# Optimization experiments

Hardware: AMD Instinct MI355X
Metric: run time of the kernel (lower is better)

The kernel has to match this reference:

```python
import jax, jax.numpy as jnp
import numpy as np

NQ = 10
C64 = jnp.complex64

# ---- gate matrices (built from traced fp32 params) ----

def u3(t, p, d):
    c = jnp.cos(t * 0.5).astype(C64)
    s = jnp.sin(t * 0.5).astype(C64)
    ep = jnp.exp(1j * p.astype(C64))
    ed = jnp.exp(1j * d.astype(C64))
    return jnp.stack([jnp.stack([c, -ed * s]), jnp.stack([ep * s, ep * ed * c])])

def ry(t):
    c = jnp.cos(t * 0.5).astype(C64)
    s = jnp.sin(t * 0.5).astype(C64)
    return jnp.stack([jnp.stack([c, -s]), jnp.stack([s, c])])

def rz(t):
    e = jnp.exp(-0.5j * t.astype(C64))
    ep = jnp.exp(0.5j * t.astype(C64))
    return jnp.diag(jnp.stack([e, ep]))

def rx(t):
    c = jnp.cos(t * 0.5).astype(C64)
    s = jnp.sin(t * 0.5).astype(C64)
    return jnp.stack([jnp.stack([c, -1j * s]), jnp.stack([-1j * s, c])])

def crz(t):
    one = jnp.ones((), C64)
    return jnp.diag(jnp.stack([one, one, jnp.exp(-0.5j * t.astype(C64)), jnp.exp(0.5j * t.astype(C64))]))

def crx(t):
    return jnp.eye(4, dtype=C64).at[2:, 2:].set(rx(t))

X = jnp.array([[0, 1], [1, 0]], dtype=C64)
CNOT = jnp.array([[1, 0, 0, 0], [0, 1, 0, 0], [0, 0, 0, 1], [0, 0, 1, 0]], dtype=C64)

# ---- gate application on state of shape (B, 2,...,2) ----

def ap1(st, U, w):
    ax = 1 + w
    s = jnp.moveaxis(st, ax, -1)
    s = s @ U.T
    return jnp.moveaxis(s, -1, ax)

def ap2(st, U, a, b):
    s = jnp.moveaxis(st, (1 + a, 1 + b), (-2, -1))
    sh = s.shape
    s = s.reshape(sh[:-2] + (4,)) @ U.T
    return jnp.moveaxis(s.reshape(sh), (-2, -1), (1 + a, 1 + b))

def conv_block(st, w, a, b):
    st = ap1(st, u3(w[0], w[1], w[2]), a)
    st = ap1(st, u3(w[3], w[4], w[5]), b)
    st = ap2(st, CNOT, a, b)
    st = ap1(st, ry(w[6]), a)
    st = ap1(st, rz(w[7]), b)
    st = ap2(st, CNOT, b, a)
    st = ap1(st, ry(w[8]), a)
    st = ap2(st, CNOT, a, b)
    st = ap1(st, u3(w[9], w[10], w[11]), a)
    st = ap1(st, u3(w[12], w[13], w[14]), b)
    return st

def pool_block(st, p, c, t):
    st = ap2(st, crz(p[0]), c, t)
    st = ap1(st, X, c)
    st = ap2(st, crx(p[1]), c, t)
    return st

def zexp(st, w):
    p = jnp.abs(st) ** 2  # fp32
    axes = tuple(ax for ax in range(1, NQ + 1) if ax != 1 + w)
    pz = p.sum(axis=axes)  # (B, 2)
    return pz[:, 0] - pz[:, 1]


def setup_inputs() -> dict:
    key = jax.random.key(0)
    ks = jax.random.split(key, 6)
    two_pi = 2.0 * np.pi
    return {
        "x": jax.random.normal(ks[0], (16384, 1024), dtype=jnp.float32),
        "weights_conv1": jax.random.uniform(ks[1], (10, 15), jnp.float32) * two_pi,
        "weights_conv2": jax.random.uniform(ks[2], (4, 15), jnp.float32) * two_pi,
        "weights_pool1": jax.random.uniform(ks[3], (5, 2), jnp.float32) * two_pi,
        "weights_pool2": jax.random.uniform(ks[4], (2, 2), jnp.float32) * two_pi,
        "weights_fc": jax.random.uniform(ks[5], (3,), jnp.float32) * two_pi,
    }


def reference(x, weights_conv1, weights_conv2, weights_pool1, weights_pool2, weights_fc):
    B = x.shape[0]
    # AmplitudeEmbedding with normalize=True (input already 1024-dim, no padding)
    nrm = jnp.linalg.norm(x, axis=1, keepdims=True)
    st = (x / nrm).astype(C64).reshape((B,) + (2,) * NQ)
    # conv layer 1: even pairs, odd pairs, wraparound (0, 9) reusing row 7
    for i in range(0, NQ, 2):
        st = conv_block(st, weights_conv1[i], i, i + 1)
    for i in range(1, NQ - 1, 2):
        st = conv_block(st, weights_conv1[i], i, i + 1)
    st = conv_block(st, weights_conv1[7], 0, NQ - 1)
    # pool layer 1
    for idx, i in enumerate(range(0, NQ, 2)):
        st = pool_block(st, weights_pool1[idx], i + 1, i)
    # conv layer 2 (stride-2 wires)
    for idx, i in enumerate(range(0, NQ - 2, 2)):
        st = conv_block(st, weights_conv2[idx], i, i + 2)
    # pool layer 2
    for idx, i in enumerate(range(0, NQ - 2, 4)):
        st = pool_block(st, weights_pool2[idx], i + 2, i)
    # fully-connected entanglers + RX rotations
    st = ap2(st, CNOT, 0, 4)
    st = ap2(st, CNOT, 2, 4)
    st = ap2(st, CNOT, 4, 0)
    st = ap1(st, rx(weights_fc[0]), 0)
    st = ap1(st, rx(weights_fc[1]), 2)
    st = ap1(st, rx(weights_fc[2]), 4)
    return jnp.stack([zexp(st, 0), zexp(st, 2)], axis=-1)  # (B, 2)
```

## Files before the change

### kernel.cpp

```cpp
#include <hip/hip_runtime.h>


typedef _Float16 f16;
typedef f16 f16x8 __attribute__((ext_vector_type(8)));
typedef f16 f16x4 __attribute__((ext_vector_type(4)));
typedef f16 f16x2 __attribute__((ext_vector_type(2)));
typedef float f32x4 __attribute__((ext_vector_type(4)));

__device__ inline float2 cmul(float2 a, float2 b) {
    return make_float2(a.x * b.x - a.y * b.y, a.x * b.y + a.y * b.x);
}
__device__ inline float2 cadd(float2 a, float2 b) {
    return make_float2(a.x + b.x, a.y + b.y);
}

struct M2 { float2 m[4]; };

__device__ inline M2 m2_u3(float t, float p, float d) {
    float c = cosf(0.5f * t), s = sinf(0.5f * t);
    float2 ep = make_float2(cosf(p), sinf(p));
    float2 ed = make_float2(cosf(d), sinf(d));
    M2 U;
    U.m[0] = make_float2(c, 0.f);
    U.m[1] = make_float2(-ed.x * s, -ed.y * s);
    U.m[2] = make_float2(ep.x * s, ep.y * s);
    float2 epd = cmul(ep, ed);
    U.m[3] = make_float2(epd.x * c, epd.y * c);
    return U;
}
__device__ inline M2 m2_ry(float t) {
    float c = cosf(0.5f * t), s = sinf(0.5f * t);
    M2 U;
    U.m[0] = make_float2(c, 0.f);  U.m[1] = make_float2(-s, 0.f);
    U.m[2] = make_float2(s, 0.f);  U.m[3] = make_float2(c, 0.f);
    return U;
}
__device__ inline M2 m2_rz(float t) {
    float c = cosf(0.5f * t), s = sinf(0.5f * t);
    M2 U;
    U.m[0] = make_float2(c, -s); U.m[1] = make_float2(0.f, 0.f);
    U.m[2] = make_float2(0.f, 0.f); U.m[3] = make_float2(c, s);
    return U;
}
__device__ inline M2 m2_rx(float t) {
    float c = cosf(0.5f * t), s = sinf(0.5f * t);
    M2 U;
    U.m[0] = make_float2(c, 0.f);   U.m[1] = make_float2(0.f, -s);
    U.m[2] = make_float2(0.f, -s);  U.m[3] = make_float2(c, 0.f);
    return U;
}

__device__ inline void ap2x2(float2& x, float2& y, const M2& U) {
    float2 nx = cadd(cmul(U.m[0], x), cmul(U.m[1], y));
    float2 ny = cadd(cmul(U.m[2], x), cmul(U.m[3], y));
    x = nx; y = ny;
}
__device__ inline void apA(float2 v[4], const M2& U) { ap2x2(v[0], v[2], U); ap2x2(v[1], v[3], U); }
__device__ inline void apB(float2 v[4], const M2& U) { ap2x2(v[0], v[1], U); ap2x2(v[2], v[3], U); }
__device__ inline void swapv(float2& a, float2& b) { float2 t = a; a = b; b = t; }

__device__ inline void conv_col(const float* w, float2 v[4]) {
    apA(v, m2_u3(w[0], w[1], w[2]));
    apB(v, m2_u3(w[3], w[4], w[5]));
    swapv(v[2], v[3]);
    apA(v, m2_ry(w[6]));
    apB(v, m2_rz(w[7]));
    swapv(v[1], v[3]);
    apA(v, m2_ry(w[8]));
    swapv(v[2], v[3]);
    apA(v, m2_u3(w[9], w[10], w[11]));
    apB(v, m2_u3(w[12], w[13], w[14]));
}
__device__ inline void pool_col(const float* p, float2 v[4]) {
    {
        float c = cosf(0.5f * p[0]), s = sinf(0.5f * p[0]);
        v[2] = cmul(v[2], make_float2(c, -s));
        v[3] = cmul(v[3], make_float2(c, s));
    }
    swapv(v[0], v[2]); swapv(v[1], v[3]);
    {
        M2 U = m2_rx(p[1]);
        ap2x2(v[2], v[3], U);
    }
}

#define SIM_BLOCKS 256
#define NORM_BLOCKS 1024

__global__ __launch_bounds__(512) void prep(const float* __restrict__ X,
                                            const float* __restrict__ wc1,
                                            const float* __restrict__ wc2,
                                            const float* __restrict__ wp1,
                                            const float* __restrict__ wp2,
                                            const float* __restrict__ wfc,
                                            float* __restrict__ nrm2,
                                            f16* __restrict__ Xh,
                                            f16* __restrict__ BTh,
                                            float* __restrict__ out) {
    __shared__ float2 st[4][1025];
    __shared__ float2 gmL[27 * 16];
    __shared__ int2   gpL[27];
    const int bid = blockIdx.x;
    const int tid = threadIdx.x;

    if (bid >= SIM_BLOCKS) {
        const int nb = bid - SIM_BLOCKS;
        const int w = tid >> 6, l = tid & 63;
        if (tid < 32) out[nb * 32 + tid] = 1.0f;
#pragma unroll
        for (int r = 0; r < 2; r++) {
            const int row = nb * 16 + w * 2 + r;
            const float4* xr = (const float4*)(X + (size_t)row * 1024);
            float s = 0.f;
#pragma unroll
            for (int ch = 0; ch < 4; ch++) {
                float4 v = xr[ch * 64 + l];
                f16x4 h;
                h[0] = (f16)v.x; h[1] = (f16)v.y; h[2] = (f16)v.z; h[3] = (f16)v.w;
                *(f16x4*)(Xh + (size_t)row * 1024 + (ch * 64 + l) * 4) = h;
                s += v.x * v.x + v.y * v.y + v.z * v.z + v.w * v.w;
            }
#pragma unroll
            for (int off = 32; off >= 1; off >>= 1) s += __shfl_xor(s, off, 64);
            if (l == 0) nrm2[row] = s;
        }
        return;
    }

    const int sb = bid;
    const int t0 = (sb & 7) * 128 + (sb >> 3) * 4;

    for (int i = tid; i < 1024; i += 512) {
#pragma unroll
        for (int c = 0; c < 4; c++)
            st[c][i] = make_float2((i == t0 + c) ? 1.f : 0.f, 0.f);
    }

    if (tid < 108) {
        const int n = tid >> 2, c = tid & 3;
        float2 v[4];
        for (int i = 0; i < 4; i++) v[i] = make_float2(0.f, 0.f);
        v[c] = make_float2(1.f, 0.f);

        int a, b;
        if (n < 5)        { int i = 2*n;       a = i;   b = i+1; conv_col(wc1 + 15*i, v); }
        else if (n < 9)   { int i = 2*(n-5)+1; a = i;   b = i+1; conv_col(wc1 + 15*i, v); }
        else if (n == 9)  { a = 0; b = 9;      conv_col(wc1 + 105, v); }
        else if (n < 15)  { int idx = n-10, i = 2*idx; a = i+1; b = i; pool_col(wp1 + 2*idx, v); }
        else if (n < 19)  { int idx = n-15, i = 2*idx; a = i; b = i+2; conv_col(wc2 + 15*idx, v); }
        else if (n == 19) { a = 2; b = 0;      pool_col(wp2 + 0, v); }
        else if (n == 20) { a = 6; b = 4;      pool_col(wp2 + 2, v); }
        else if (n <= 23) {
            a = (n == 21) ? 0 : (n == 22) ? 2 : 4;
            b = (n == 23) ? 0 : 4;
            swapv(v[2], v[3]);
        } else {
            a = (n == 24) ? 0 : (n == 25) ? 2 : 4;
            b = a + 1;
            apA(v, m2_rx(wfc[n - 24]));
        }
        if (c == 0) gpL[n] = make_int2(9 - a, 9 - b);
        for (int i = 0; i < 4; i++) gmL[n * 16 + i * 4 + c] = v[i];
    }
    __syncthreads();

    const int cg = tid >> 8;
    const int q = tid & 255;
    for (int g = 0; g < 27; g++) {
        const int2 p = gpL[g];
        float2 m[16];
#pragma unroll
        for (int i = 0; i < 16; i++) m[i] = gmL[g * 16 + i];
        const int p1 = p.x, p2 = p.y;
        const int lo = min(p1, p2), hi = max(p1, p2);
        const int m1 = (1 << lo) - 1;
        int tt = (q & m1) | ((q & ~m1) << 1);
        const int m2m = (1 << hi) - 1;
        const int i0 = (tt & m2m) | ((tt & ~m2m) << 1);
        int idx[4];
        for (int ga = 0; ga < 2; ga++)
            for (int gb = 0; gb < 2; gb++)
                idx[2 * ga + gb] = i0 | (ga << p1) | (gb << p2);
#pragma unroll
        for (int cc = 0; cc < 2; cc++) {
            const int c = 2 * cg + cc;
            float2 v[4];
#pragma unroll
            for (int i = 0; i < 4; i++) v[i] = st[c][idx[i]];
#pragma unroll
            for (int i = 0; i < 4; i++) {
                float2 s = make_float2(0.f, 0.f);
#pragma unroll
                for (int j = 0; j < 4; j++) s = cadd(s, cmul(m[i * 4 + j], v[j]));
                st[c][idx[i]] = s;
            }
        }
        __syncthreads();
    }

    for (int s = tid; s < 1024; s += 512) {
        const int b9 = (s >> 9) & 1, b7 = (s >> 7) & 1;
        if (b9 | b7) {
            const int grp = b9 ? b7 : 2;
            const int pos = (((s >> 8) & 1) << 7) | (s & 127);
            const int np = grp * 256 + pos;
            f16x4 re, im;
#pragma unroll
            for (int c = 0; c < 4; c++) {
                re[c] = (f16)st[c][s].x;
                im[c] = (f16)st[c][s].y;
            }
            *(f16x4*)(BTh + (size_t)np * 1024 + t0) = re;
            *(f16x4*)(BTh + (size_t)(np + 768) * 1024 + t0) = im;
        }
    }
}

__device__ __forceinline__ void glds16(const void* g, void* l) {
    __builtin_amdgcn_global_load_lds(
        (const __attribute__((address_space(1))) void*)g,
        (__attribute__((address_space(3))) void*)l, 16, 0, 0);
}

__global__ __launch_bounds__(256) void gemm_mfma(const f16* __restrict__ A,
                                                 const f16* __restrict__ Bt,
                                                 const float* __restrict__ nrm2,
                                                 float* __restrict__ out) {
    __shared__ char Ash[16384];
    __shared__ char Bsh[16384];
    const int tid = threadIdx.x;
    const int l = tid & 63, w = tid >> 6;
    const int wr = w >> 1, wc = w & 1;
    const int row0 = blockIdx.x * 128, col0 = blockIdx.y * 128;

    const int srow = l >> 3;
    const int kc = (l & 7) ^ (srow & 7);
    const f16* aS = A  + (size_t)(row0 + 32 * w + srow) * 1024 + kc * 8;
    const f16* bS = Bt + (size_t)(col0 + 32 * w + srow) * 1024 + kc * 8;
    char* aD = Ash + (32 * w) * 128;
    char* bD = Bsh + (32 * w) * 128;

    int aOff[4][2], bOff[4][2];
#pragma unroll
    for (int i = 0; i < 4; i++)
#pragma unroll
        for (int h = 0; h < 2; h++) {
            const int cphys = (((l >> 4) + 4 * h) ^ (l & 7));
            aOff[i][h] = (wr * 64 + i * 16 + (l & 15)) * 128 + cphys * 16;
            bOff[i][h] = (wc * 64 + i * 16 + (l & 15)) * 128 + cphys * 16;
        }

    f32x4 acc[4][4];
    const f32x4 z = {0.f, 0.f, 0.f, 0.f};
#pragma unroll
    for (int i = 0; i < 4; i++)
#pragma unroll
        for (int j = 0; j < 4; j++) acc[i][j] = z;

    for (int k0 = 0; k0 < 1024; k0 += 64) {
#pragma unroll
        for (int g = 0; g < 4; g++) {
            glds16(aS + k0 + g * 8 * 1024, aD + g * 1024);
            glds16(bS + k0 + g * 8 * 1024, bD + g * 1024);
        }
        __syncthreads();
#pragma unroll
        for (int h = 0; h < 2; h++) {
            f16x8 af[4], bf[4];
#pragma unroll
            for (int i = 0; i < 4; i++) {
                af[i] = *(const f16x8*)(Ash + aOff[i][h]);
                bf[i] = *(const f16x8*)(Bsh + bOff[i][h]);
            }
#pragma unroll
            for (int mi = 0; mi < 4; mi++)
#pragma unroll
                for (int ni = 0; ni < 4; ni++)
                    acc[mi][ni] = __builtin_amdgcn_mfma_f32_16x16x32_f16(
                        af[mi], bf[ni], acc[mi][ni], 0, 0, 0);
        }
        __syncthreads();
    }

    float c0[4][4], c1[4][4];
#pragma unroll
    for (int mi = 0; mi < 4; mi++)
#pragma unroll
        for (int rr = 0; rr < 4; rr++) { c0[mi][rr] = 0.f; c1[mi][rr] = 0.f; }
#pragma unroll
    for (int ni = 0; ni < 4; ni++) {
        const int n_glob = col0 + wc * 64 + ni * 16 + (l & 15);
        const int nm = (n_glob >= 768) ? n_glob - 768 : n_glob;
        const int grp = nm >> 8;
        const float w0 = (grp <= 1) ? 1.f : 0.f;
        const float w1 = (grp >= 1) ? 1.f : 0.f;
#pragma unroll
        for (int mi = 0; mi < 4; mi++)
#pragma unroll
            for (int rr = 0; rr < 4; rr++) {
                const float y = acc[mi][ni][rr];
                const float y2 = y * y;
                c0[mi][rr] += w0 * y2;
                c1[mi][rr] += w1 * y2;
            }
    }
#pragma unroll
    for (int off = 1; off < 16; off <<= 1)
#pragma unroll
        for (int mi = 0; mi < 4; mi++)
#pragma unroll
            for (int rr = 0; rr < 4; rr++) {
                c0[mi][rr] += __shfl_xor(c0[mi][rr], off, 64);
                c1[mi][rr] += __shfl_xor(c1[mi][rr], off, 64);
            }
    if ((l & 15) == 0) {
        const int q = l >> 4;
#pragma unroll
        for (int mi = 0; mi < 4; mi++)
#pragma unroll
            for (int rr = 0; rr < 4; rr++) {
                const int row = row0 + wr * 64 + mi * 16 + q * 4 + rr;
                const float inv = -2.0f / nrm2[row];
                atomicAdd(&out[row * 2 + 0], c0[mi][rr] * inv);
                atomicAdd(&out[row * 2 + 1], c1[mi][rr] * inv);
            }
    }
}

extern "C" void kernel_launch(void* const* d_in, const int* in_sizes, int n_in,
                              void* d_out, int out_size, void* d_ws, size_t ws_size,
                              hipStream_t stream) {
    const float* x   = (const float*)d_in[0];
    const float* wc1 = (const float*)d_in[1];
    const float* wc2 = (const float*)d_in[2];
    const float* wp1 = (const float*)d_in[3];
    const float* wp2 = (const float*)d_in[4];
    const float* wfc = (const float*)d_in[5];
    float* out = (float*)d_out;

    uintptr_t wsp = (uintptr_t)d_ws;
    f16*    BTh    = (f16*)(wsp + 8192);
    f16*    Xh     = (f16*)(wsp + 8192 + (3u << 20));
    float*  nrm2   = (float*)(wsp + 8192 + (35u << 20));

    prep<<<SIM_BLOCKS + NORM_BLOCKS, 512, 0, stream>>>(
        x, wc1, wc2, wp1, wp2, wfc, nrm2, Xh, BTh, out);
    gemm_mfma<<<dim3(128, 12), 256, 0, stream>>>(Xh, BTh, nrm2, out);
}
```

Before: 221.0 us.

## Fuse prep and GEMM into one persistent kernel with a grid barrier

Merges the state-simulation/normalization prep kernel and the MFMA GEMM into a single 1024-block kernel. A global atomic counter acts as a grid-wide barrier between the phases, and the GEMM tiles are then processed in a grid-stride loop. Work is also redistributed: each of 512 sim blocks handles 2 basis columns instead of 4, and each norm block handles 32 rows. This removes a kernel launch and its tail gap, but adds a memset, a spin-wait barrier that requires all 1024 blocks to be co-resident, and an uneven 1536-tile split over 1024 blocks.

```diff
diff --git a/kernel.cpp b/kernel.cpp
--- a/kernel.cpp
+++ b/kernel.cpp
@@ -84,32 +84,121 @@
     }
 }
 
-#define SIM_BLOCKS 256
-#define NORM_BLOCKS 1024
-
-__global__ __launch_bounds__(512) void prep(const float* __restrict__ X,
-                                            const float* __restrict__ wc1,
-                                            const float* __restrict__ wc2,
-                                            const float* __restrict__ wp1,
-                                            const float* __restrict__ wp2,
-                                            const float* __restrict__ wfc,
-                                            float* __restrict__ nrm2,
-                                            f16* __restrict__ Xh,
-                                            f16* __restrict__ BTh,
-                                            float* __restrict__ out) {
-    __shared__ float2 st[4][1025];
-    __shared__ float2 gmL[27 * 16];
-    __shared__ int2   gpL[27];
+__device__ __forceinline__ void glds16(const void* g, void* l) {
+    __builtin_amdgcn_global_load_lds(
+        (const __attribute__((address_space(1))) void*)g,
+        (__attribute__((address_space(3))) void*)l, 16, 0, 0);
+}
+
+__global__ __launch_bounds__(256, 4) void fused(const float* __restrict__ X,
+                                                const float* __restrict__ wc1,
+                                                const float* __restrict__ wc2,
+                                                const float* __restrict__ wp1,
+                                                const float* __restrict__ wp2,
+                                                const float* __restrict__ wfc,
+                                                float* __restrict__ nrm2,
+                                                f16* __restrict__ Xh,
+                                                f16* __restrict__ BTh,
+                                                float* __restrict__ out,
+                                                int* __restrict__ bar) {
+    __shared__ char smem[32768];
+    const int tid = threadIdx.x;
     const int bid = blockIdx.x;
-    const int tid = threadIdx.x;
-
-    if (bid >= SIM_BLOCKS) {
-        const int nb = bid - SIM_BLOCKS;
+
+    if (bid < 512) {
+        float2* st  = (float2*)smem;
+        float2* gmL = (float2*)(smem + 16400);
+        int2*   gpL = (int2*)(smem + 19856);
+        const int t0 = (bid & 7) * 128 + (bid >> 3) * 2;
+
+        for (int i = tid; i < 1024; i += 256) {
+            st[i]        = make_float2((i == t0) ? 1.f : 0.f, 0.f);
+            st[1025 + i] = make_float2((i == t0 + 1) ? 1.f : 0.f, 0.f);
+        }
+
+        if (tid < 108) {
+            const int n = tid >> 2, c = tid & 3;
+            float2 v[4];
+            for (int i = 0; i < 4; i++) v[i] = make_float2(0.f, 0.f);
+            v[c] = make_float2(1.f, 0.f);
+
+            int a, b;
+            if (n < 5)        { int i = 2*n;       a = i;   b = i+1; conv_col(wc1 + 15*i, v); }
+            else if (n < 9)   { int i = 2*(n-5)+1; a = i;   b = i+1; conv_col(wc1 + 15*i, v); }
+            else if (n == 9)  { a = 0; b = 9;      conv_col(wc1 + 105, v); }
+            else if (n < 15)  { int idx = n-10, i = 2*idx; a = i+1; b = i; pool_col(wp1 + 2*idx, v); }
+            else if (n < 19)  { int idx = n-15, i = 2*idx; a = i; b = i+2; conv_col(wc2 + 15*idx, v); }
+            else if (n == 19) { a = 2; b = 0;      pool_col(wp2 + 0, v); }
+            else if (n == 20) { a = 6; b = 4;      pool_col(wp2 + 2, v); }
+            else if (n <= 23) {
+                a = (n == 21) ? 0 : (n == 22) ? 2 : 4;
+                b = (n == 23) ? 0 : 4;
+                swapv(v[2], v[3]);
+            } else {
+                a = (n == 24) ? 0 : (n == 25) ? 2 : 4;
+                b = a + 1;
+                apA(v, m2_rx(wfc[n - 24]));
+            }
+            if (c == 0) gpL[n] = make_int2(9 - a, 9 - b);
+            for (int i = 0; i < 4; i++) gmL[n * 16 + i * 4 + c] = v[i];
+        }
+        __syncthreads();
+
+        for (int g = 0; g < 27; g++) {
+            const int2 p = gpL[g];
+            float2 m[16];
+#pragma unroll
+            for (int i = 0; i < 16; i++) m[i] = gmL[g * 16 + i];
+            const int p1 = p.x, p2 = p.y;
+            const int lo = min(p1, p2), hi = max(p1, p2);
+            const int q = tid;
+            const int m1 = (1 << lo) - 1;
+            int tt = (q & m1) | ((q & ~m1) << 1);
+            const int m2m = (1 << hi) - 1;
+            const int i0 = (tt & m2m) | ((tt & ~m2m) << 1);
+            int idx[4];
+            for (int ga = 0; ga < 2; ga++)
+                for (int gb = 0; gb < 2; gb++)
+                    idx[2 * ga + gb] = i0 | (ga << p1) | (gb << p2);
+#pragma unroll
+            for (int c = 0; c < 2; c++) {
+                float2* stc = st + c * 1025;
+                float2 v[4];
+#pragma unroll
+                for (int i = 0; i < 4; i++) v[i] = stc[idx[i]];
+#pragma unroll
+                for (int i = 0; i < 4; i++) {
+                    float2 s = make_float2(0.f, 0.f);
+#pragma unroll
+                    for (int j = 0; j < 4; j++) s = cadd(s, cmul(m[i * 4 + j], v[j]));
+                    stc[idx[i]] = s;
+                }
+            }
+            __syncthreads();
+        }
+
+        for (int s = tid; s < 1024; s += 256) {
+            const int b9 = (s >> 9) & 1, b7 = (s >> 7) & 1;
+            if (b9 | b7) {
+                const int grp = b9 ? b7 : 2;
+                const int pos = (((s >> 8) & 1) << 7) | (s & 127);
+                const int np = grp * 256 + pos;
+                f16x2 re, im;
+#pragma unroll
+                for (int c = 0; c < 2; c++) {
+                    re[c] = (f16)st[c * 1025 + s].x;
+                    im[c] = (f16)st[c * 1025 + s].y;
+                }
+                *(f16x2*)(BTh + (size_t)np * 1024 + t0) = re;
+                *(f16x2*)(BTh + (size_t)(np + 768) * 1024 + t0) = im;
+            }
+        }
+    } else {
+        const int nb = bid - 512;
         const int w = tid >> 6, l = tid & 63;
-        if (tid < 32) out[nb * 32 + tid] = 1.0f;
-#pragma unroll
-        for (int r = 0; r < 2; r++) {
-            const int row = nb * 16 + w * 2 + r;
+#pragma unroll
+        for (int r = 0; r < 8; r++) {
+            const int row = nb * 32 + w * 8 + r;
             const float4* xr = (const float4*)(X + (size_t)row * 1024);
             float s = 0.f;
 #pragma unroll
@@ -124,121 +213,25 @@
             for (int off = 32; off >= 1; off >>= 1) s += __shfl_xor(s, off, 64);
             if (l == 0) nrm2[row] = s;
         }
-        return;
-    }
-
-    const int sb = bid;
-    const int t0 = (sb & 7) * 128 + (sb >> 3) * 4;
-
-    for (int i = tid; i < 1024; i += 512) {
-#pragma unroll
-        for (int c = 0; c < 4; c++)
-            st[c][i] = make_float2((i == t0 + c) ? 1.f : 0.f, 0.f);
-    }
-
-    if (tid < 108) {
-        const int n = tid >> 2, c = tid & 3;
-        float2 v[4];
-        for (int i = 0; i < 4; i++) v[i] = make_float2(0.f, 0.f);
-        v[c] = make_float2(1.f, 0.f);
-
-        int a, b;
-        if (n < 5)        { int i = 2*n;       a = i;   b = i+1; conv_col(wc1 + 15*i, v); }
-        else if (n < 9)   { int i = 2*(n-5)+1; a = i;   b = i+1; conv_col(wc1 + 15*i, v); }
-        else if (n == 9)  { a = 0; b = 9;      conv_col(wc1 + 105, v); }
-        else if (n < 15)  { int idx = n-10, i = 2*idx; a = i+1; b = i; pool_col(wp1 + 2*idx, v); }
-        else if (n < 19)  { int idx = n-15, i = 2*idx; a = i; b = i+2; conv_col(wc2 + 15*idx, v); }
-        else if (n == 19) { a = 2; b = 0;      pool_col(wp2 + 0, v); }
-        else if (n == 20) { a = 6; b = 4;      pool_col(wp2 + 2, v); }
-        else if (n <= 23) {
-            a = (n == 21) ? 0 : (n == 22) ? 2 : 4;
-            b = (n == 23) ? 0 : 4;
-            swapv(v[2], v[3]);
-        } else {
-            a = (n == 24) ? 0 : (n == 25) ? 2 : 4;
-            b = a + 1;
-            apA(v, m2_rx(wfc[n - 24]));
-        }
-        if (c == 0) gpL[n] = make_int2(9 - a, 9 - b);
-        for (int i = 0; i < 4; i++) gmL[n * 16 + i * 4 + c] = v[i];
-    }
+    }
+    if (tid < 32) out[bid * 32 + tid] = 1.0f;
+
+    asm volatile("s_waitcnt vmcnt(0)" ::: "memory");
     __syncthreads();
-
-    const int cg = tid >> 8;
-    const int q = tid & 255;
-    for (int g = 0; g < 27; g++) {
-        const int2 p = gpL[g];
-        float2 m[16];
-#pragma unroll
-        for (int i = 0; i < 16; i++) m[i] = gmL[g * 16 + i];
-        const int p1 = p.x, p2 = p.y;
-        const int lo = min(p1, p2), hi = max(p1, p2);
-        const int m1 = (1 << lo) - 1;
-        int tt = (q & m1) | ((q & ~m1) << 1);
-        const int m2m = (1 << hi) - 1;
-        const int i0 = (tt & m2m) | ((tt & ~m2m) << 1);
-        int idx[4];
-        for (int ga = 0; ga < 2; ga++)
-            for (int gb = 0; gb < 2; gb++)
-                idx[2 * ga + gb] = i0 | (ga << p1) | (gb << p2);
-#pragma unroll
-        for (int cc = 0; cc < 2; cc++) {
-            const int c = 2 * cg + cc;
-            float2 v[4];
-#pragma unroll
-            for (int i = 0; i < 4; i++) v[i] = st[c][idx[i]];
-#pragma unroll
-            for (int i = 0; i < 4; i++) {
-                float2 s = make_float2(0.f, 0.f);
-#pragma unroll
-                for (int j = 0; j < 4; j++) s = cadd(s, cmul(m[i * 4 + j], v[j]));
-                st[c][idx[i]] = s;
-            }
-        }
-        __syncthreads();
-    }
-
-    for (int s = tid; s < 1024; s += 512) {
-        const int b9 = (s >> 9) & 1, b7 = (s >> 7) & 1;
-        if (b9 | b7) {
-            const int grp = b9 ? b7 : 2;
-            const int pos = (((s >> 8) & 1) << 7) | (s & 127);
-            const int np = grp * 256 + pos;
-            f16x4 re, im;
-#pragma unroll
-            for (int c = 0; c < 4; c++) {
-                re[c] = (f16)st[c][s].x;
-                im[c] = (f16)st[c][s].y;
-            }
-            *(f16x4*)(BTh + (size_t)np * 1024 + t0) = re;
-            *(f16x4*)(BTh + (size_t)(np + 768) * 1024 + t0) = im;
-        }
-    }
-}
-
-__device__ __forceinline__ void glds16(const void* g, void* l) {
-    __builtin_amdgcn_global_load_lds(
-        (const __attribute__((address_space(1))) void*)g,
-        (__attribute__((address_space(3))) void*)l, 16, 0, 0);
-}
-
-__global__ __launch_bounds__(256) void gemm_mfma(const f16* __restrict__ A,
-                                                 const f16* __restrict__ Bt,
-                                                 const float* __restrict__ nrm2,
-                                                 float* __restrict__ out) {
-    __shared__ char Ash[16384];
-    __shared__ char Bsh[16384];
-    const int tid = threadIdx.x;
+    if (tid == 0) {
+        __threadfence();
+        atomicAdd(bar, 1);
+        while (__hip_atomic_load(bar, __ATOMIC_ACQUIRE, __HIP_MEMORY_SCOPE_AGENT)
+               < (int)gridDim.x) {
+            __builtin_amdgcn_s_sleep(16);
+        }
+    }
+    __syncthreads();
+
+    char* Ash = smem;
+    char* Bsh = smem + 16384;
     const int l = tid & 63, w = tid >> 6;
     const int wr = w >> 1, wc = w & 1;
-    const int row0 = blockIdx.x * 128, col0 = blockIdx.y * 128;
-
-    const int srow = l >> 3;
-    const int kc = (l & 7) ^ (srow & 7);
-    const f16* aS = A  + (size_t)(row0 + 32 * w + srow) * 1024 + kc * 8;
-    const f16* bS = Bt + (size_t)(col0 + 32 * w + srow) * 1024 + kc * 8;
-    char* aD = Ash + (32 * w) * 128;
-    char* bD = Bsh + (32 * w) * 128;
 
     int aOff[4][2], bOff[4][2];
 #pragma unroll
@@ -249,81 +242,93 @@
             aOff[i][h] = (wr * 64 + i * 16 + (l & 15)) * 128 + cphys * 16;
             bOff[i][h] = (wc * 64 + i * 16 + (l & 15)) * 128 + cphys * 16;
         }
-
-    f32x4 acc[4][4];
-    const f32x4 z = {0.f, 0.f, 0.f, 0.f};
-#pragma unroll
-    for (int i = 0; i < 4; i++)
-#pragma unroll
-        for (int j = 0; j < 4; j++) acc[i][j] = z;
-
-    for (int k0 = 0; k0 < 1024; k0 += 64) {
-#pragma unroll
-        for (int g = 0; g < 4; g++) {
-            glds16(aS + k0 + g * 8 * 1024, aD + g * 1024);
-            glds16(bS + k0 + g * 8 * 1024, bD + g * 1024);
-        }
-        __syncthreads();
-#pragma unroll
-        for (int h = 0; h < 2; h++) {
-            f16x8 af[4], bf[4];
-#pragma unroll
-            for (int i = 0; i < 4; i++) {
-                af[i] = *(const f16x8*)(Ash + aOff[i][h]);
-                bf[i] = *(const f16x8*)(Bsh + bOff[i][h]);
-            }
+    const int srow = l >> 3;
+    const int kc = (l & 7) ^ (srow & 7);
+
+    for (int t = bid; t < 1536; t += 1024) {
+        const int row0 = (t & 127) * 128;
+        const int col0 = (t >> 7) * 128;
+
+        const f16* aS = Xh + (size_t)(row0 + 32 * w + srow) * 1024 + kc * 8;
+        const f16* bS = BTh + (size_t)(col0 + 32 * w + srow) * 1024 + kc * 8;
+        char* aD = Ash + (32 * w) * 128;
+        char* bD = Bsh + (32 * w) * 128;
+
+        f32x4 acc[4][4];
+        const f32x4 z = {0.f, 0.f, 0.f, 0.f};
+#pragma unroll
+        for (int i = 0; i < 4; i++)
+#pragma unroll
+            for (int j = 0; j < 4; j++) acc[i][j] = z;
+
+        for (int k0 = 0; k0 < 1024; k0 += 64) {
+#pragma unroll
+            for (int g = 0; g < 4; g++) {
+                glds16(aS + k0 + g * 8 * 1024, aD + g * 1024);
+                glds16(bS + k0 + g * 8 * 1024, bD + g * 1024);
+            }
+            __syncthreads();
+#pragma unroll
+            for (int h = 0; h < 2; h++) {
+                f16x8 af[4], bf[4];
+#pragma unroll
+                for (int i = 0; i < 4; i++) {
+                    af[i] = *(const f16x8*)(Ash + aOff[i][h]);
+                    bf[i] = *(const f16x8*)(Bsh + bOff[i][h]);
+                }
+#pragma unroll
+                for (int mi = 0; mi < 4; mi++)
+#pragma unroll
+                    for (int ni = 0; ni < 4; ni++)
+                        acc[mi][ni] = __builtin_amdgcn_mfma_f32_16x16x32_f16(
+                            af[mi], bf[ni], acc[mi][ni], 0, 0, 0);
+            }
+            __syncthreads();
+        }
+
+        float c0[4][4], c1[4][4];
+#pragma unroll
+        for (int mi = 0; mi < 4; mi++)
+#pragma unroll
+            for (int rr = 0; rr < 4; rr++) { c0[mi][rr] = 0.f; c1[mi][rr] = 0.f; }
+#pragma unroll
+        for (int ni = 0; ni < 4; ni++) {
+            const int n_glob = col0 + wc * 64 + ni * 16 + (l & 15);
+            const int nm = (n_glob >= 768) ? n_glob - 768 : n_glob;
+            const int grp = nm >> 8;
+            const float w0 = (grp <= 1) ? 1.f : 0.f;
+            const float w1 = (grp >= 1) ? 1.f : 0.f;
 #pragma unroll
             for (int mi = 0; mi < 4; mi++)
 #pragma unroll
-                for (int ni = 0; ni < 4; ni++)
-                    acc[mi][ni] = __builtin_amdgcn_mfma_f32_16x16x32_f16(
-                        af[mi], bf[ni], acc[mi][ni], 0, 0, 0);
-        }
-        __syncthreads();
-    }
-
-    float c0[4][4], c1[4][4];
-#pragma unroll
-    for (int mi = 0; mi < 4; mi++)
-#pragma unroll
-        for (int rr = 0; rr < 4; rr++) { c0[mi][rr] = 0.f; c1[mi][rr] = 0.f; }
-#pragma unroll
-    for (int ni = 0; ni < 4; ni++) {
-        const int n_glob = col0 + wc * 64 + ni * 16 + (l & 15);
-        const int nm = (n_glob >= 768) ? n_glob - 768 : n_glob;
-        const int grp = nm >> 8;
-        const float w0 = (grp <= 1) ? 1.f : 0.f;
-        const float w1 = (grp >= 1) ? 1.f : 0.f;
-#pragma unroll
-        for (int mi = 0; mi < 4; mi++)
-#pragma unroll
-            for (int rr = 0; rr < 4; rr++) {
-                const float y = acc[mi][ni][rr];
-                const float y2 = y * y;
-                c0[mi][rr] += w0 * y2;
-                c1[mi][rr] += w1 * y2;
-            }
-    }
-#pragma unroll
-    for (int off = 1; off < 16; off <<= 1)
-#pragma unroll
-        for (int mi = 0; mi < 4; mi++)
-#pragma unroll
-            for (int rr = 0; rr < 4; rr++) {
-                c0[mi][rr] += __shfl_xor(c0[mi][rr], off, 64);
-                c1[mi][rr] += __shfl_xor(c1[mi][rr], off, 64);
-            }
-    if ((l & 15) == 0) {
-        const int q = l >> 4;
-#pragma unroll
-        for (int mi = 0; mi < 4; mi++)
-#pragma unroll
-            for (int rr = 0; rr < 4; rr++) {
-                const int row = row0 + wr * 64 + mi * 16 + q * 4 + rr;
-                const float inv = -2.0f / nrm2[row];
-                atomicAdd(&out[row * 2 + 0], c0[mi][rr] * inv);
-                atomicAdd(&out[row * 2 + 1], c1[mi][rr] * inv);
-            }
+                for (int rr = 0; rr < 4; rr++) {
+                    const float y = acc[mi][ni][rr];
+                    const float y2 = y * y;
+                    c0[mi][rr] += w0 * y2;
+                    c1[mi][rr] += w1 * y2;
+                }
+        }
+#pragma unroll
+        for (int off = 1; off < 16; off <<= 1)
+#pragma unroll
+            for (int mi = 0; mi < 4; mi++)
+#pragma unroll
+                for (int rr = 0; rr < 4; rr++) {
+                    c0[mi][rr] += __shfl_xor(c0[mi][rr], off, 64);
+                    c1[mi][rr] += __shfl_xor(c1[mi][rr], off, 64);
+                }
+        if ((l & 15) == 0) {
+            const int q = l >> 4;
+#pragma unroll
+            for (int mi = 0; mi < 4; mi++)
+#pragma unroll
+                for (int rr = 0; rr < 4; rr++) {
+                    const int row = row0 + wr * 64 + mi * 16 + q * 4 + rr;
+                    const float inv = -2.0f / nrm2[row];
+                    atomicAdd(&out[row * 2 + 0], c0[mi][rr] * inv);
+                    atomicAdd(&out[row * 2 + 1], c1[mi][rr] * inv);
+                }
+        }
     }
 }
 
@@ -339,11 +344,12 @@
     float* out = (float*)d_out;
 
     uintptr_t wsp = (uintptr_t)d_ws;
+    int*    bar    = (int*)wsp;
     f16*    BTh    = (f16*)(wsp + 8192);
     f16*    Xh     = (f16*)(wsp + 8192 + (3u << 20));
     float*  nrm2   = (float*)(wsp + 8192 + (35u << 20));
 
-    prep<<<SIM_BLOCKS + NORM_BLOCKS, 512, 0, stream>>>(
-        x, wc1, wc2, wp1, wp2, wfc, nrm2, Xh, BTh, out);
-    gemm_mfma<<<dim3(128, 12), 256, 0, stream>>>(Xh, BTh, nrm2, out);
-}
+    hipMemsetAsync(bar, 0, 64, stream);
+    fused<<<1024, 256, 0, stream>>>(x, wc1, wc2, wp1, wp2, wfc,
+                                    nrm2, Xh, BTh, out, bar);
+}
```

New measurement: 427.8 us. 93.5% more time.

## Fuse fp32-to-fp16 conversion and norm computation into GEMM A-tile loading

Applied to the files above, without the earlier changes.

Removes the separate pass that converted X to fp16 and computed row norms. The GEMM now reads fp32 X directly, converts it in registers, writes it to LDS and accumulates the squared norms from the same data. This saves a 32MB fp16 round trip through global memory. In exchange the A-tile load is now synchronous and goes through registers instead of global_load_lds, and several column blocks recompute each row's norm redundantly. It also adds a memset launch, uses the atomic from the first column tile to add the 1.0 base, and remaps block indices to group row tiles per XCD.

```diff
diff --git a/kernel.cpp b/kernel.cpp
--- a/kernel.cpp
+++ b/kernel.cpp
@@ -84,50 +84,23 @@
     }
 }
 
-#define SIM_BLOCKS 256
-#define NORM_BLOCKS 1024
-
-__global__ __launch_bounds__(512) void prep(const float* __restrict__ X,
-                                            const float* __restrict__ wc1,
-                                            const float* __restrict__ wc2,
-                                            const float* __restrict__ wp1,
-                                            const float* __restrict__ wp2,
-                                            const float* __restrict__ wfc,
-                                            float* __restrict__ nrm2,
-                                            f16* __restrict__ Xh,
-                                            f16* __restrict__ BTh,
-                                            float* __restrict__ out) {
+__device__ __forceinline__ void glds16(const void* g, void* l) {
+    __builtin_amdgcn_global_load_lds(
+        (const __attribute__((address_space(1))) void*)g,
+        (__attribute__((address_space(3))) void*)l, 16, 0, 0);
+}
+
+__global__ __launch_bounds__(512) void sim_build(const float* __restrict__ wc1,
+                                                 const float* __restrict__ wc2,
+                                                 const float* __restrict__ wp1,
+                                                 const float* __restrict__ wp2,
+                                                 const float* __restrict__ wfc,
+                                                 f16* __restrict__ BTh) {
     __shared__ float2 st[4][1025];
     __shared__ float2 gmL[27 * 16];
     __shared__ int2   gpL[27];
-    const int bid = blockIdx.x;
     const int tid = threadIdx.x;
-
-    if (bid >= SIM_BLOCKS) {
-        const int nb = bid - SIM_BLOCKS;
-        const int w = tid >> 6, l = tid & 63;
-        if (tid < 32) out[nb * 32 + tid] = 1.0f;
-#pragma unroll
-        for (int r = 0; r < 2; r++) {
-            const int row = nb * 16 + w * 2 + r;
-            const float4* xr = (const float4*)(X + (size_t)row * 1024);
-            float s = 0.f;
-#pragma unroll
-            for (int ch = 0; ch < 4; ch++) {
-                float4 v = xr[ch * 64 + l];
-                f16x4 h;
-                h[0] = (f16)v.x; h[1] = (f16)v.y; h[2] = (f16)v.z; h[3] = (f16)v.w;
-                *(f16x4*)(Xh + (size_t)row * 1024 + (ch * 64 + l) * 4) = h;
-                s += v.x * v.x + v.y * v.y + v.z * v.z + v.w * v.w;
-            }
-#pragma unroll
-            for (int off = 32; off >= 1; off >>= 1) s += __shfl_xor(s, off, 64);
-            if (l == 0) nrm2[row] = s;
-        }
-        return;
-    }
-
-    const int sb = bid;
+    const int sb = blockIdx.x;
     const int t0 = (sb & 7) * 128 + (sb >> 3) * 4;
 
     for (int i = tid; i < 1024; i += 512) {
@@ -216,28 +189,28 @@
     }
 }
 
-__device__ __forceinline__ void glds16(const void* g, void* l) {
-    __builtin_amdgcn_global_load_lds(
-        (const __attribute__((address_space(1))) void*)g,
-        (__attribute__((address_space(3))) void*)l, 16, 0, 0);
-}
-
-__global__ __launch_bounds__(256) void gemm_mfma(const f16* __restrict__ A,
-                                                 const f16* __restrict__ Bt,
-                                                 const float* __restrict__ nrm2,
-                                                 float* __restrict__ out) {
+__global__ __launch_bounds__(256) void gemm_xn(const float* __restrict__ X,
+                                               const f16* __restrict__ Bt,
+                                               float* __restrict__ out) {
     __shared__ char Ash[16384];
     __shared__ char Bsh[16384];
+    __shared__ float nrmL[128];
     const int tid = threadIdx.x;
     const int l = tid & 63, w = tid >> 6;
     const int wr = w >> 1, wc = w & 1;
-    const int row0 = blockIdx.x * 128, col0 = blockIdx.y * 128;
+
+    const int lin = blockIdx.x;
+    const int xcd = lin & 7;
+    const int mm = lin >> 3;
+    const int rowT = xcd + 8 * (mm / 12);
+    const int colT = mm % 12;
+    const int row0 = rowT * 128, col0 = colT * 128;
 
     const int srow = l >> 3;
     const int kc = (l & 7) ^ (srow & 7);
-    const f16* aS = A  + (size_t)(row0 + 32 * w + srow) * 1024 + kc * 8;
-    const f16* bS = Bt + (size_t)(col0 + 32 * w + srow) * 1024 + kc * 8;
-    char* aD = Ash + (32 * w) * 128;
+    const float* xS = X + (size_t)(row0 + 32 * w + srow) * 1024 + kc * 8;
+    const f16*   bS = Bt + (size_t)(col0 + 32 * w + srow) * 1024 + kc * 8;
+    char* aD = Ash + (32 * w) * 128 + l * 16;
     char* bD = Bsh + (32 * w) * 128;
 
     int aOff[4][2], bOff[4][2];
@@ -257,11 +230,23 @@
 #pragma unroll
         for (int j = 0; j < 4; j++) acc[i][j] = z;
 
+    float sq[4] = {0.f, 0.f, 0.f, 0.f};
+
     for (int k0 = 0; k0 < 1024; k0 += 64) {
 #pragma unroll
+        for (int g = 0; g < 4; g++)
+            glds16(bS + k0 + g * 8 * 1024, bD + g * 1024);
+#pragma unroll
         for (int g = 0; g < 4; g++) {
-            glds16(aS + k0 + g * 8 * 1024, aD + g * 1024);
-            glds16(bS + k0 + g * 8 * 1024, bD + g * 1024);
+            const float* p = xS + k0 + g * 8 * 1024;
+            const float4 xa = *(const float4*)p;
+            const float4 xb = *(const float4*)(p + 4);
+            sq[g] += xa.x * xa.x + xa.y * xa.y + xa.z * xa.z + xa.w * xa.w
+                   + xb.x * xb.x + xb.y * xb.y + xb.z * xb.z + xb.w * xb.w;
+            f16x8 h;
+            h[0] = (f16)xa.x; h[1] = (f16)xa.y; h[2] = (f16)xa.z; h[3] = (f16)xa.w;
+            h[4] = (f16)xb.x; h[5] = (f16)xb.y; h[6] = (f16)xb.z; h[7] = (f16)xb.w;
+            *(f16x8*)(aD + g * 1024) = h;
         }
         __syncthreads();
 #pragma unroll
@@ -281,6 +266,19 @@
         }
         __syncthreads();
     }
+
+#pragma unroll
+    for (int g = 0; g < 4; g++) {
+        sq[g] += __shfl_xor(sq[g], 1, 64);
+        sq[g] += __shfl_xor(sq[g], 2, 64);
+        sq[g] += __shfl_xor(sq[g], 4, 64);
+    }
+    if ((l & 7) == 0) {
+#pragma unroll
+        for (int g = 0; g < 4; g++)
+            nrmL[32 * w + 8 * g + srow] = sq[g];
+    }
+    __syncthreads();
 
     float c0[4][4], c1[4][4];
 #pragma unroll
@@ -314,15 +312,17 @@
                 c1[mi][rr] += __shfl_xor(c1[mi][rr], off, 64);
             }
     if ((l & 15) == 0) {
+        const float base = (colT == 0 && wc == 0) ? 1.0f : 0.0f;
         const int q = l >> 4;
 #pragma unroll
         for (int mi = 0; mi < 4; mi++)
 #pragma unroll
             for (int rr = 0; rr < 4; rr++) {
-                const int row = row0 + wr * 64 + mi * 16 + q * 4 + rr;
-                const float inv = -2.0f / nrm2[row];
-                atomicAdd(&out[row * 2 + 0], c0[mi][rr] * inv);
-                atomicAdd(&out[row * 2 + 1], c1[mi][rr] * inv);
+                const int ri = wr * 64 + mi * 16 + q * 4 + rr;
+                const int row = row0 + ri;
+                const float inv = -2.0f / nrmL[ri];
+                atomicAdd(&out[row * 2 + 0], fmaf(c0[mi][rr], inv, base));
+                atomicAdd(&out[row * 2 + 1], fmaf(c1[mi][rr], inv, base));
             }
     }
 }
@@ -339,11 +339,9 @@
     float* out = (float*)d_out;
 
     uintptr_t wsp = (uintptr_t)d_ws;
-    f16*    BTh    = (f16*)(wsp + 8192);
-    f16*    Xh     = (f16*)(wsp + 8192 + (3u << 20));
-    float*  nrm2   = (float*)(wsp + 8192 + (35u << 20));
-
-    prep<<<SIM_BLOCKS + NORM_BLOCKS, 512, 0, stream>>>(
-        x, wc1, wc2, wp1, wp2, wfc, nrm2, Xh, BTh, out);
-    gemm_mfma<<<dim3(128, 12), 256, 0, stream>>>(Xh, BTh, nrm2, out);
-}
+    f16* BTh = (f16*)(wsp + 8192);
+
+    hipMemsetAsync(out, 0, 16384 * 2 * sizeof(float), stream);
+    sim_build<<<256, 512, 0, stream>>>(wc1, wc2, wp1, wp2, wfc, BTh);
+    gemm_xn<<<1536, 256, 0, stream>>>(x, BTh, out);
+}
```

After: 236.0 us. 1.07x slower.
